# Performance work log

Measured on AMD Instinct MI355X. Metric: run time of the kernel, lower is better.

The kernel has to match this reference:

```python
import jax, jax.numpy as jnp
import numpy as np

B, T, V, S = 16, 1000, 4096, 100
NEG = -1e30  # log-space 'zero' (avoid actual -inf for numerical safety)


def setup_inputs() -> dict:
    key = jax.random.key(0)
    k1, k2, k3, k4 = jax.random.split(key, 4)
    outputs_pred = jax.random.normal(k1, (B, T, V), dtype=jnp.float32)
    y = jax.random.randint(k2, (B, S), 1, V)          # labels in [1, V-1]; 0 is blank
    f_len = jax.random.randint(k3, (B,), T // 2, T + 1)
    y_len = jax.random.randint(k4, (B,), S // 2, S + 1)
    return {"outputs_pred": outputs_pred, "y": y, "f_len": f_len, "y_len": y_len}


def _ctc_losses(log_probs, y, f_len, y_len):
    # log_probs: [B,T,V]; y: [B,S]; returns per-example neg log-likelihood [B]
    Bb, Tt, Vv = log_probs.shape
    Ss = y.shape[1]
    L = 2 * Ss + 1  # extended label sequence length (blanks interleaved)
    # extended labels: z[2i]=blank(0), z[2i+1]=y[i]
    z = jnp.zeros((Bb, L), dtype=y.dtype).at[:, 1::2].set(y)
    # gather label log-probs for every time step: [B,T,L]
    lp_z = jnp.take_along_axis(log_probs, jnp.broadcast_to(z[:, None, :], (Bb, Tt, L)), axis=2)
    # skip transition s-2 -> s allowed iff z[s] != blank and z[s] != z[s-2]
    z_prev2 = jnp.pad(z, ((0, 0), (2, 0)), constant_values=-1)[:, :L]
    allow_skip = (z != 0) & (z != z_prev2)  # [B,L]

    alpha0 = jnp.full((Bb, L), NEG, dtype=log_probs.dtype)
    alpha0 = alpha0.at[:, 0].set(lp_z[:, 0, 0]).at[:, 1].set(lp_z[:, 0, 1])

    def step(alpha, inputs):
        lp_t, t = inputs  # lp_t: [B,L]
        a1 = alpha
        a2 = jnp.pad(alpha, ((0, 0), (1, 0)), constant_values=NEG)[:, :L]
        a3 = jnp.pad(alpha, ((0, 0), (2, 0)), constant_values=NEG)[:, :L]
        a3 = jnp.where(allow_skip, a3, NEG)
        m = jnp.maximum(jnp.maximum(a1, a2), a3)
        lse = m + jnp.log(jnp.exp(a1 - m) + jnp.exp(a2 - m) + jnp.exp(a3 - m))
        new = lse + lp_t
        # freeze alpha for finished sequences (t >= f_len)
        new = jnp.where((t < f_len)[:, None], new, alpha)
        return new, None

    lp_z_t = jnp.swapaxes(lp_z, 0, 1)  # [T,B,L]
    alpha, _ = jax.lax.scan(step, alpha0, (lp_z_t[1:], jnp.arange(1, Tt)))

    idx1 = 2 * y_len                      # final blank position
    idx2 = jnp.maximum(2 * y_len - 1, 0)  # final label position
    a1 = jnp.take_along_axis(alpha, idx1[:, None], axis=1)[:, 0]
    a2 = jnp.take_along_axis(alpha, idx2[:, None], axis=1)[:, 0]
    loss = -jnp.logaddexp(a1, a2)
    # zero_infinity=True: zero out (pseudo-)infinite losses
    loss = jnp.where(loss < 1e29, loss, 0.0)
    return loss


def reference(outputs_pred, y, f_len, y_len):
    log_probs = jax.nn.log_softmax(outputs_pred, axis=-1)
    return _ctc_losses(log_probs, y, f_len, y_len).mean()
```

## Files before the change

kernel.cpp:

```cpp
#include <hip/hip_runtime.h>
#include <hip/hip_bf16.h>

#define LN2D 0.6931471805599453

constexpr int Bc = 16, Tc = 1000, Vc = 4096, Sc = 100;
constexpr int TP = Tc / 2;
constexpr int NCHUNK = 32;

__device__ __forceinline__ double dpp_wshr1_f64(double x) {
  int lo = __double2loint(x), hi = __double2hiint(x);
  lo = __builtin_amdgcn_update_dpp(0, lo, 0x138, 0xF, 0xF, false);
  hi = __builtin_amdgcn_update_dpp(0, hi, 0x138, 0xF, 0xF, false);
  return __hiloint2double(hi, lo);
}
__device__ __forceinline__ double dpp_wshl1_f64(double x) {
  int lo = __double2loint(x), hi = __double2hiint(x);
  lo = __builtin_amdgcn_update_dpp(0, lo, 0x130, 0xF, 0xF, false);
  hi = __builtin_amdgcn_update_dpp(0, hi, 0x130, 0xF, 0xF, false);
  return __hiloint2double(hi, lo);
}

#define ACQ_FENCE() __builtin_amdgcn_fence(__ATOMIC_ACQUIRE, "agent")

__device__ __forceinline__ void st_bf16_coherent(__hip_bfloat16* p, float v) {
  __hip_bfloat16 h = __float2bfloat16(v);
  unsigned short us = __builtin_bit_cast(unsigned short, h);
  __hip_atomic_store((unsigned short*)p, us, __ATOMIC_RELAXED,
                     __HIP_MEMORY_SCOPE_AGENT);
}

__global__ __launch_bounds__(64) void k_zero(unsigned int* __restrict__ prog) {
  for (int k = threadIdx.x; k < Bc * NCHUNK; k += 64) prog[k] = 0u;
}

__global__ __launch_bounds__(256) void k_fused(
    const float* __restrict__ x, const int* __restrict__ y,
    const int* __restrict__ f_len, const int* __restrict__ y_len,
    __hip_bfloat16* __restrict__ pp, unsigned int* __restrict__ prog,
    double* __restrict__ aw, double* __restrict__ bw,
    int* __restrict__ Kf, int* __restrict__ Kb)
{
  if (blockIdx.x >= 2 * Bc) {
    int j = (int)blockIdx.x - 2 * Bc;
    int b = j & 15, r = j >> 4;
    int F = f_len[b];
    if (r >= F) return;
    int t = (r & 1) ? (F - 1 - (r >> 1)) : (r >> 1);
    int tid = threadIdx.x;
    __shared__ float sh[Vc];
    __shared__ float red[8];
    const float4* row4 = (const float4*)(x + ((size_t)b * Tc + t) * Vc);
    float4* sh4 = (float4*)sh;
    float4 v[4];
    float mx = -3.4e38f;
#pragma unroll
    for (int k = 0; k < 4; ++k) {
      v[k] = row4[k * 256 + tid];
      sh4[k * 256 + tid] = v[k];
      mx = fmaxf(mx, fmaxf(fmaxf(v[k].x, v[k].y), fmaxf(v[k].z, v[k].w)));
    }
#pragma unroll
    for (int off = 32; off; off >>= 1) mx = fmaxf(mx, __shfl_xor(mx, off));
    if ((tid & 63) == 0) red[tid >> 6] = mx;
    __syncthreads();
    mx = fmaxf(fmaxf(red[0], red[1]), fmaxf(red[2], red[3]));
    float s = 0.f;
#pragma unroll
    for (int k = 0; k < 4; ++k) {
      s += __expf(v[k].x - mx) + __expf(v[k].y - mx) +
           __expf(v[k].z - mx) + __expf(v[k].w - mx);
    }
#pragma unroll
    for (int off = 32; off; off >>= 1) s += __shfl_xor(s, off);
    if ((tid & 63) == 0) red[4 + (tid >> 6)] = s;
    __syncthreads();
    s = (red[4] + red[5]) + (red[6] + red[7]);
    float lse = mx + __logf(s);
    float p;
    if (tid <= 200) {
      int lab = (tid & 1) ? y[b * Sc + (tid >> 1)] : 0;
      p = __expf(sh[lab] - lse);
    } else {
      p = 0.f;
    }
    st_bf16_coherent(
        pp + (size_t)b * (TP * 512) + (size_t)(t >> 1) * 512 + tid * 2 + (t & 1),
        p);
    __syncthreads();
    if (tid == 0)
      __hip_atomic_fetch_add(&prog[b * NCHUNK + (t >> 5)], 1u,
                             __ATOMIC_RELAXED, __HIP_MEMORY_SCOPE_AGENT);
    return;
  }
  if (threadIdx.x >= 64) return;
  int b = blockIdx.x >> 1;
  int dir = blockIdx.x & 1;
  int lane = threadIdx.x;
  const uint4* pbp = (const uint4*)(pp + (size_t)b * (TP * 512));
  int F = f_len[b];
  int mid = F >> 1;
  const int* yb = y + b * Sc;
  int i0 = 2 * lane, i1i = 2 * lane + 1;
  int y_m1 = (i0 >= 1 && i0 - 1 < Sc) ? yb[i0 - 1] : -1;
  int y_0  = (i0 < Sc) ? yb[i0] : -2;
  int y_1  = (i1i < Sc) ? yb[i1i] : -3;
  bool allow1 = (y_0 != y_m1);
  bool allow3 = (y_1 != y_0);
  int K = 0;

  ACQ_FENCE();

#define LODW(W) ((double)__int_as_float((int)((W) << 16)))
#define HIDW(W) ((double)__int_as_float((int)((W) & 0xffff0000u)))
#define RORMAXI(M, CTRL)                                                      \
  {                                                                           \
    int _t = __builtin_amdgcn_update_dpp(0, (M), (CTRL), 0xF, 0xF, false);    \
    (M) = (_t > (M)) ? _t : (M);                                              \
  }
#define EXPC(c) ((F - 32 * (c)) < 32 ? (unsigned)(F - 32 * (c)) : 32u)
#define SPIN_ON(c)                                                            \
  {                                                                           \
    while (__hip_atomic_load(&prog[b * NCHUNK + (c)], __ATOMIC_RELAXED,       \
                             __HIP_MEMORY_SCOPE_AGENT) < EXPC(c)) {           \
      __builtin_amdgcn_s_sleep(8);                                            \
    }                                                                         \
  }

  if (dir == 0) {
    int E = mid + 1;
    int maxpf = (E - 1) >> 1;
    int cwm = -1;
#define WAITF(c)                                                              \
  {                                                                           \
    int _c = (c);                                                             \
    if (_c > cwm) {                                                           \
      for (int cc = cwm + 1; cc <= _c; ++cc) SPIN_ON(cc);                     \
      cwm = _c;                                                               \
    }                                                                         \
  }

    WAITF((2 * ((16 < maxpf) ? 16 : maxpf) + 1) >> 5);
    uint4 u0 = pbp[lane];
    double a0 = (lane == 0) ? LODW(u0.x) : 0.0;
    double a1 = (lane == 0) ? LODW(u0.y) : 0.0;
    double a2 = 0.0, a3 = 0.0;
    double un = 0.0;

#define SC(PX, PY, PZ, PW)                                                    \
  {                                                                           \
    double u = (lane == 0) ? 0.0 : un;                                        \
    double n0 = (a0 + u) * (PX);                                              \
    double n1 = (a1 + a0 + (allow1 ? u : 0.0)) * (PY);                        \
    double n2 = (a2 + a1) * (PZ);                                             \
    double n3 = (a3 + a2 + (allow3 ? a1 : 0.0)) * (PW);                       \
    un = dpp_wshr1_f64(n3);                                                   \
    a0 = n0; a1 = n1; a2 = n2; a3 = n3;                                       \
  }
#define LOADPF(B, T)                                                          \
  {                                                                           \
    int tt = (T); tt = tt < maxpf ? tt : maxpf;                               \
    B = pbp[(size_t)tt * 64 + lane];                                          \
  }
#define PAIRP(B, TN)                                                          \
  {                                                                           \
    uint4 c = B; LOADPF(B, TN);                                               \
    SC(LODW(c.x), LODW(c.y), LODW(c.z), LODW(c.w));                           \
    SC(HIDW(c.x), HIDW(c.y), HIDW(c.z), HIDW(c.w));                           \
  }
#define TPAIR(B)                                                              \
  if (2 * k < E) {                                                            \
    uint4 c = B;                                                              \
    SC(LODW(c.x), LODW(c.y), LODW(c.z), LODW(c.w));                           \
    if (2 * k + 1 < E) { SC(HIDW(c.x), HIDW(c.y), HIDW(c.z), HIDW(c.w)); }    \
    ++k;                                                                      \
  }
#define RESCALE_F                                                             \
  {                                                                           \
    int _h = max(max(__double2hiint(a0), __double2hiint(a1)),                 \
                 max(__double2hiint(a2), __double2hiint(a3)));                \
    RORMAXI(_h, 0x121); RORMAXI(_h, 0x122);                                   \
    RORMAXI(_h, 0x124); RORMAXI(_h, 0x128);                                   \
    int _g = max(max(__builtin_amdgcn_readlane(_h, 0),                        \
                     __builtin_amdgcn_readlane(_h, 16)),                      \
                 max(__builtin_amdgcn_readlane(_h, 32),                       \
                     __builtin_amdgcn_readlane(_h, 48)));                     \
    int _e = (_g >> 20) - 1279;                                               \
    double _sc = __hiloint2double((1023 - _e) << 20, 0);                      \
    a0 *= _sc; a1 *= _sc; a2 *= _sc; a3 *= _sc; un *= _sc;                    \
    K -= _e;                                                                  \
  }

    SC(HIDW(u0.x), HIDW(u0.y), HIDW(u0.z), HIDW(u0.w));

    uint4 b0, b1, b2, b3, b4, b5, b6, b7, b8, b9, b10, b11, b12, b13, b14, b15;
    LOADPF(b0, 1);   LOADPF(b1, 2);   LOADPF(b2, 3);   LOADPF(b3, 4);
    LOADPF(b4, 5);   LOADPF(b5, 6);   LOADPF(b6, 7);   LOADPF(b7, 8);
    LOADPF(b8, 9);   LOADPF(b9, 10);  LOADPF(b10, 11); LOADPF(b11, 12);
    LOADPF(b12, 13); LOADPF(b13, 14); LOADPF(b14, 15); LOADPF(b15, 16);

    int k = 1;
    for (; 2 * k + 32 <= E; k += 16) {
      int pfh = (k + 31 < maxpf) ? (k + 31) : maxpf;
      WAITF((2 * pfh + 1) >> 5);
      PAIRP(b0, k + 16); PAIRP(b1, k + 17); PAIRP(b2, k + 18); PAIRP(b3, k + 19);
      PAIRP(b4, k + 20); PAIRP(b5, k + 21); PAIRP(b6, k + 22); PAIRP(b7, k + 23);
      RESCALE_F;
      PAIRP(b8, k + 24);  PAIRP(b9, k + 25);  PAIRP(b10, k + 26); PAIRP(b11, k + 27);
      PAIRP(b12, k + 28); PAIRP(b13, k + 29); PAIRP(b14, k + 30); PAIRP(b15, k + 31);
      RESCALE_F;
    }
    TPAIR(b0); TPAIR(b1); TPAIR(b2); TPAIR(b3);
    TPAIR(b4); TPAIR(b5); TPAIR(b6); TPAIR(b7);
    RESCALE_F;
    TPAIR(b8);  TPAIR(b9);  TPAIR(b10); TPAIR(b11);
    TPAIR(b12); TPAIR(b13); TPAIR(b14); TPAIR(b15);

    double* A = aw + b * 256 + 4 * lane;
    A[0] = a0; A[1] = a1; A[2] = a2; A[3] = a3;
    if (lane == 0) Kf[b] = K;
  } else {
    int stop = mid + 1;
    int minpb = stop >> 1;
    int cwmB = ((F - 1) >> 5) + 1;
#define WAITB(c)                                                              \
  {                                                                           \
    int _c = (c);                                                             \
    if (_c < cwmB) {                                                          \
      for (int cc = cwmB - 1; cc >= _c; --cc) SPIN_ON(cc);                    \
      cwmB = _c;                                                              \
    }                                                                         \
  }

    int yl = y_len[b];
    int idx1 = 2 * yl;
    int idx2 = (2 * yl - 1 > 0) ? (2 * yl - 1) : 0;
    int s0 = 4 * lane;
    double bb0 = (s0 == idx1 || s0 == idx2) ? 1.0 : 0.0;
    double bb1 = (s0 + 1 == idx1 || s0 + 1 == idx2) ? 1.0 : 0.0;
    double bb2 = (s0 + 2 == idx1 || s0 + 2 == idx2) ? 1.0 : 0.0;
    double bb3 = (s0 + 3 == idx1 || s0 + 3 == idx2) ? 1.0 : 0.0;

#define BC(PX, PY, PZ, PW)                                                    \
  {                                                                           \
    double t0 = bb0 * (PX), t1 = bb1 * (PY);                                  \
    double t2 = bb2 * (PZ), t3 = bb3 * (PW);                                  \
    double q = t0 + (allow1 ? t1 : 0.0);                                      \
    double qs = dpp_wshl1_f64(q);                                             \
    bb0 = t0 + t1;                                                            \
    bb1 = t1 + t2 + (allow3 ? t3 : 0.0);                                      \
    bb2 = t2 + t3;                                                            \
    bb3 = t3 + qs;                                                            \
  }
#define LOADPB(B, T)                                                          \
  {                                                                           \
    int tt = (T); tt = tt > minpb ? tt : minpb;                               \
    B = pbp[(size_t)tt * 64 + lane];                                          \
  }
#define BPAIRP(B, TN)                                                         \
  {                                                                           \
    uint4 c = B; LOADPB(B, TN);                                               \
    BC(HIDW(c.x), HIDW(c.y), HIDW(c.z), HIDW(c.w));                           \
    BC(LODW(c.x), LODW(c.y), LODW(c.z), LODW(c.w));                           \
  }
#define BTPAIR(B)                                                             \
  {                                                                           \
    uint4 c = B;                                                              \
    if (2 * kb + 1 >= stop) { BC(HIDW(c.x), HIDW(c.y), HIDW(c.z), HIDW(c.w)); } \
    if (2 * kb >= stop) { BC(LODW(c.x), LODW(c.y), LODW(c.z), LODW(c.w)); }   \
    --kb;                                                                     \
  }
#define RESCALE_B                                                             \
  {                                                                           \
    int _h = max(max(__double2hiint(bb0), __double2hiint(bb1)),               \
                 max(__double2hiint(bb2), __double2hiint(bb3)));              \
    RORMAXI(_h, 0x121); RORMAXI(_h, 0x122);                                   \
    RORMAXI(_h, 0x124); RORMAXI(_h, 0x128);                                   \
    int _g = max(max(__builtin_amdgcn_readlane(_h, 0),                        \
                     __builtin_amdgcn_readlane(_h, 16)),                      \
                 max(__builtin_amdgcn_readlane(_h, 32),                       \
                     __builtin_amdgcn_readlane(_h, 48)));                     \
    int _e = (_g >> 20) - 1279;                                               \
    double _sc = __hiloint2double((1023 - _e) << 20, 0);                      \
    bb0 *= _sc; bb1 *= _sc; bb2 *= _sc; bb3 *= _sc;                           \
    K -= _e;                                                                  \
  }

    int kb = (F - 1) >> 1;
    WAITB((F - 1) >> 5);
    if (((F - 1) & 1) == 0) {
      uint4 c = pbp[(size_t)kb * 64 + lane];
      BC(LODW(c.x), LODW(c.y), LODW(c.z), LODW(c.w));
      --kb;
    }
    {
      int pl0 = (kb - 15 > minpb) ? (kb - 15) : minpb;
      WAITB((2 * pl0) >> 5);
    }
    uint4 c0, c1, c2, c3, c4, c5, c6, c7, c8, c9, c10, c11, c12, c13, c14, c15;
    LOADPB(c0, kb);       LOADPB(c1, kb - 1);   LOADPB(c2, kb - 2);   LOADPB(c3, kb - 3);
    LOADPB(c4, kb - 4);   LOADPB(c5, kb - 5);   LOADPB(c6, kb - 6);   LOADPB(c7, kb - 7);
    LOADPB(c8, kb - 8);   LOADPB(c9, kb - 9);   LOADPB(c10, kb - 10); LOADPB(c11, kb - 11);
    LOADPB(c12, kb - 12); LOADPB(c13, kb - 13); LOADPB(c14, kb - 14); LOADPB(c15, kb - 15);

    for (; 2 * (kb - 15) >= stop; kb -= 16) {
      int pfl = (kb - 31 > minpb) ? (kb - 31) : minpb;
      WAITB((2 * pfl) >> 5);
      BPAIRP(c0, kb - 16); BPAIRP(c1, kb - 17); BPAIRP(c2, kb - 18); BPAIRP(c3, kb - 19);
      BPAIRP(c4, kb - 20); BPAIRP(c5, kb - 21); BPAIRP(c6, kb - 22); BPAIRP(c7, kb - 23);
      RESCALE_B;
      BPAIRP(c8, kb - 24);  BPAIRP(c9, kb - 25);  BPAIRP(c10, kb - 26); BPAIRP(c11, kb - 27);
      BPAIRP(c12, kb - 28); BPAIRP(c13, kb - 29); BPAIRP(c14, kb - 30); BPAIRP(c15, kb - 31);
      RESCALE_B;
    }
    BTPAIR(c0); BTPAIR(c1); BTPAIR(c2); BTPAIR(c3);
    BTPAIR(c4); BTPAIR(c5); BTPAIR(c6); BTPAIR(c7);
    RESCALE_B;
    BTPAIR(c8);  BTPAIR(c9);  BTPAIR(c10); BTPAIR(c11);
    BTPAIR(c12); BTPAIR(c13); BTPAIR(c14); BTPAIR(c15);

    double* Bp = bw + b * 256 + 4 * lane;
    Bp[0] = bb0; Bp[1] = bb1; Bp[2] = bb2; Bp[3] = bb3;
    if (lane == 0) Kb[b] = K;
  }
}

__global__ __launch_bounds__(1024) void k_combine(
    const double* __restrict__ aw, const double* __restrict__ bw,
    const int* __restrict__ Kf, const int* __restrict__ Kb,
    float* __restrict__ out)
{
  int w = threadIdx.x >> 6, lane = threadIdx.x & 63;
  const double* A = aw + w * 256 + 4 * lane;
  const double* Bv = bw + w * 256 + 4 * lane;
  double s = A[0] * Bv[0] + A[1] * Bv[1] + A[2] * Bv[2] + A[3] * Bv[3];
#pragma unroll
  for (int off = 32; off; off >>= 1) s += __shfl_xor(s, off);
  __shared__ float sl[16];
  if (lane == 0) {
    double loss = ((double)(Kf[w] + Kb[w]) - log2(s)) * LN2D;
    float lf = (float)loss;
    if (!(lf < 1e29f)) lf = 0.f;
    sl[w] = lf;
  }
  __syncthreads();
  if (threadIdx.x < 64) {
    float v = (lane < 16) ? sl[lane] : 0.f;
#pragma unroll
    for (int off = 32; off; off >>= 1) v += __shfl_xor(v, off);
    if (lane == 0) out[0] = v / (float)Bc;
  }
}

extern "C" void kernel_launch(void* const* d_in, const int* in_sizes, int n_in,
                              void* d_out, int out_size, void* d_ws, size_t ws_size,
                              hipStream_t stream) {
  const float* x = (const float*)d_in[0];
  const int* y = (const int*)d_in[1];
  const int* f_len = (const int*)d_in[2];
  const int* y_len = (const int*)d_in[3];
  float* out = (float*)d_out;

  __hip_bfloat16* pp = (__hip_bfloat16*)d_ws;
  double* aw = (double*)((char*)d_ws + 8192000);
  double* bw = (double*)((char*)d_ws + 8224768);
  int* Kf = (int*)((char*)d_ws + 8257536);
  int* Kb = (int*)((char*)d_ws + 8257600);
  unsigned int* prog = (unsigned int*)((char*)d_ws + 8257664);

  k_zero<<<dim3(1), dim3(64), 0, stream>>>(prog);
  k_fused<<<dim3(2 * Bc + Bc * Tc), dim3(256), 0, stream>>>(
      x, y, f_len, y_len, pp, prog, aw, bw, Kf, Kb);
  k_combine<<<dim3(1), dim3(1024), 0, stream>>>(aw, bw, Kf, Kb, out);
}
```

Before: 61.13 us.

## Fold combine kernel into fused kernel via last-block-done counter and per-wave progress

Removes the separate combine kernel launch by having each recurrence wave atomically bump a done counter, with the last finisher computing the mean loss. The producer blocks now drop the block barrier and have each wave signal progress after draining its own stores, so expected counts are scaled by four. The spin sleep is also shortened. This trades a kernel launch and a block barrier for more atomics and a serialized final reduction in one wave.

```diff
diff --git a/kernel.cpp b/kernel.cpp
--- a/kernel.cpp
+++ b/kernel.cpp
@@ -21,6 +21,7 @@
 }
 
 #define ACQ_FENCE() __builtin_amdgcn_fence(__ATOMIC_ACQUIRE, "agent")
+#define VM_DRAIN() asm volatile("s_waitcnt vmcnt(0)" ::: "memory")
 
 __device__ __forceinline__ void st_bf16_coherent(__hip_bfloat16* p, float v) {
   __hip_bfloat16 h = __float2bfloat16(v);
@@ -30,7 +31,7 @@
 }
 
 __global__ __launch_bounds__(64) void k_zero(unsigned int* __restrict__ prog) {
-  for (int k = threadIdx.x; k < Bc * NCHUNK; k += 64) prog[k] = 0u;
+  for (int k = threadIdx.x; k < Bc * NCHUNK + 1; k += 64) prog[k] = 0u;
 }
 
 __global__ __launch_bounds__(256) void k_fused(
@@ -38,8 +39,9 @@
     const int* __restrict__ f_len, const int* __restrict__ y_len,
     __hip_bfloat16* __restrict__ pp, unsigned int* __restrict__ prog,
     double* __restrict__ aw, double* __restrict__ bw,
-    int* __restrict__ Kf, int* __restrict__ Kb)
+    int* __restrict__ Kf, int* __restrict__ Kb, float* __restrict__ out)
 {
+  unsigned int* done = prog + Bc * NCHUNK;
   if (blockIdx.x >= 2 * Bc) {
     int j = (int)blockIdx.x - 2 * Bc;
     int b = j & 15, r = j >> 4;
@@ -86,8 +88,8 @@
     st_bf16_coherent(
         pp + (size_t)b * (TP * 512) + (size_t)(t >> 1) * 512 + tid * 2 + (t & 1),
         p);
-    __syncthreads();
-    if (tid == 0)
+    VM_DRAIN();
+    if ((tid & 63) == 0)
       __hip_atomic_fetch_add(&prog[b * NCHUNK + (t >> 5)], 1u,
                              __ATOMIC_RELAXED, __HIP_MEMORY_SCOPE_AGENT);
     return;
@@ -117,12 +119,12 @@
     int _t = __builtin_amdgcn_update_dpp(0, (M), (CTRL), 0xF, 0xF, false);    \
     (M) = (_t > (M)) ? _t : (M);                                              \
   }
-#define EXPC(c) ((F - 32 * (c)) < 32 ? (unsigned)(F - 32 * (c)) : 32u)
+#define EXPC(c) (4u * ((F - 32 * (c)) < 32 ? (unsigned)(F - 32 * (c)) : 32u))
 #define SPIN_ON(c)                                                            \
   {                                                                           \
     while (__hip_atomic_load(&prog[b * NCHUNK + (c)], __ATOMIC_RELAXED,       \
                              __HIP_MEMORY_SCOPE_AGENT) < EXPC(c)) {           \
-      __builtin_amdgcn_s_sleep(8);                                            \
+      __builtin_amdgcn_s_sleep(2);                                            \
     }                                                                         \
   }
 
@@ -216,8 +218,12 @@
     TPAIR(b12); TPAIR(b13); TPAIR(b14); TPAIR(b15);
 
     double* A = aw + b * 256 + 4 * lane;
-    A[0] = a0; A[1] = a1; A[2] = a2; A[3] = a3;
-    if (lane == 0) Kf[b] = K;
+    __hip_atomic_store(&A[0], a0, __ATOMIC_RELAXED, __HIP_MEMORY_SCOPE_AGENT);
+    __hip_atomic_store(&A[1], a1, __ATOMIC_RELAXED, __HIP_MEMORY_SCOPE_AGENT);
+    __hip_atomic_store(&A[2], a2, __ATOMIC_RELAXED, __HIP_MEMORY_SCOPE_AGENT);
+    __hip_atomic_store(&A[3], a3, __ATOMIC_RELAXED, __HIP_MEMORY_SCOPE_AGENT);
+    if (lane == 0)
+      __hip_atomic_store(&Kf[b], K, __ATOMIC_RELAXED, __HIP_MEMORY_SCOPE_AGENT);
   } else {
     int stop = mid + 1;
     int minpb = stop >> 1;
@@ -319,35 +325,37 @@
     BTPAIR(c12); BTPAIR(c13); BTPAIR(c14); BTPAIR(c15);
 
     double* Bp = bw + b * 256 + 4 * lane;
-    Bp[0] = bb0; Bp[1] = bb1; Bp[2] = bb2; Bp[3] = bb3;
-    if (lane == 0) Kb[b] = K;
-  }
-}
-
-__global__ __launch_bounds__(1024) void k_combine(
-    const double* __restrict__ aw, const double* __restrict__ bw,
-    const int* __restrict__ Kf, const int* __restrict__ Kb,
-    float* __restrict__ out)
-{
-  int w = threadIdx.x >> 6, lane = threadIdx.x & 63;
-  const double* A = aw + w * 256 + 4 * lane;
-  const double* Bv = bw + w * 256 + 4 * lane;
-  double s = A[0] * Bv[0] + A[1] * Bv[1] + A[2] * Bv[2] + A[3] * Bv[3];
-#pragma unroll
-  for (int off = 32; off; off >>= 1) s += __shfl_xor(s, off);
-  __shared__ float sl[16];
-  if (lane == 0) {
-    double loss = ((double)(Kf[w] + Kb[w]) - log2(s)) * LN2D;
-    float lf = (float)loss;
-    if (!(lf < 1e29f)) lf = 0.f;
-    sl[w] = lf;
-  }
-  __syncthreads();
-  if (threadIdx.x < 64) {
-    float v = (lane < 16) ? sl[lane] : 0.f;
-#pragma unroll
-    for (int off = 32; off; off >>= 1) v += __shfl_xor(v, off);
-    if (lane == 0) out[0] = v / (float)Bc;
+    __hip_atomic_store(&Bp[0], bb0, __ATOMIC_RELAXED, __HIP_MEMORY_SCOPE_AGENT);
+    __hip_atomic_store(&Bp[1], bb1, __ATOMIC_RELAXED, __HIP_MEMORY_SCOPE_AGENT);
+    __hip_atomic_store(&Bp[2], bb2, __ATOMIC_RELAXED, __HIP_MEMORY_SCOPE_AGENT);
+    __hip_atomic_store(&Bp[3], bb3, __ATOMIC_RELAXED, __HIP_MEMORY_SCOPE_AGENT);
+    if (lane == 0)
+      __hip_atomic_store(&Kb[b], K, __ATOMIC_RELAXED, __HIP_MEMORY_SCOPE_AGENT);
+  }
+
+  VM_DRAIN();
+  unsigned int prev = 0;
+  if (lane == 0)
+    prev = __hip_atomic_fetch_add(done, 1u, __ATOMIC_RELAXED,
+                                  __HIP_MEMORY_SCOPE_AGENT);
+  prev = __shfl(prev, 0);
+  if (prev == 2u * Bc - 1u) {
+    ACQ_FENCE();
+    float accf = 0.f;
+    for (int bb = 0; bb < Bc; ++bb) {
+      const double* A = aw + bb * 256 + 4 * lane;
+      const double* Bv = bw + bb * 256 + 4 * lane;
+      double s = A[0] * Bv[0] + A[1] * Bv[1] + A[2] * Bv[2] + A[3] * Bv[3];
+#pragma unroll
+      for (int off = 32; off; off >>= 1) s += __shfl_xor(s, off);
+      if (lane == 0) {
+        double loss = ((double)(Kf[bb] + Kb[bb]) - log2(s)) * LN2D;
+        float lf = (float)loss;
+        if (!(lf < 1e29f)) lf = 0.f;
+        accf += lf;
+      }
+    }
+    if (lane == 0) out[0] = accf / (float)Bc;
   }
 }
 
@@ -369,6 +377,5 @@
 
   k_zero<<<dim3(1), dim3(64), 0, stream>>>(prog);
   k_fused<<<dim3(2 * Bc + Bc * Tc), dim3(256), 0, stream>>>(
-      x, y, f_len, y_len, pp, prog, aw, bw, Kf, Kb);
-  k_combine<<<dim3(1), dim3(1024), 0, stream>>>(aw, bw, Kf, Kb, out);
-}
+      x, y, f_len, y_len, pp, prog, aw, bw, Kf, Kb, out);
+}
```

Result: slower. 88.30 us (+44.5%).
